# Optimization experiments

Measured on AMD Instinct MI355X. Metric: run time of the kernel, lower is better.

Reference implementation:

```python
import jax, jax.numpy as jnp
import numpy as np

N, H, W = 131072, 28, 28


def _mute(x):
    """Vectorized mute_bit: m,e = frexp(x); e = 0 if e > 1 else e; ldexp(m, e).
    Equivalent to scaling x by 2**(-e) when e > 1, identity otherwise.
    frexp's integer exponent carries no gradient, so this is also vjp-safe."""
    e = jnp.frexp(x)[1]                      # integer exponent, frexp convention: x = m * 2**e, m in [0.5,1)
    shift = jnp.where(e > 1, -e, 0).astype(x.dtype)
    return x * jnp.exp2(shift)


def setup_inputs() -> dict:
    key = jax.random.key(0)
    kx, = jax.random.split(key, 1)
    # scale by 8 so a substantial fraction of elements have exponent > 1 (mute path fires)
    x = jax.random.normal(kx, (N, H, W), dtype=jnp.float32) * 8.0
    rows = jnp.array([0, 7, 14, 21], dtype=jnp.int32)
    cols = jnp.array([3, 10, 17, 24], dtype=jnp.int32)
    return {"x": x, "rows": rows, "cols": cols}


def reference(x, rows, cols):
    # Mute selected full rows first (X[i][r][j] for j in 0..27), then selected full cols
    # (X[i][j][c] for j in 0..27) on the already-updated array, matching loop order.
    x = x.at[:, rows, :].set(_mute(x[:, rows, :]))
    x = x.at[:, :, cols].set(_mute(x[:, :, cols]))
    return x
```

## Files before the change

### kernel.cpp

```cpp
#include <hip/hip_runtime.h>

__device__ __forceinline__ float mute1(float v) {
    unsigned b = __float_as_uint(v);
    unsigned e = (b >> 23) & 0xffu;
    float m = __uint_as_float((b & 0x807FFFFFu) | 0x3F000000u);
    return (e >= 128u) ? m : v;
}

__global__ __launch_bounds__(256) void mute_kernel(
    const float4* __restrict__ x, float4* __restrict__ out,
    const int* __restrict__ rows, const int* __restrict__ cols, int n4)
{
    unsigned row_mask = (1u << rows[0]) | (1u << rows[1]) | (1u << rows[2]) | (1u << rows[3]);
    unsigned col_mask = (1u << cols[0]) | (1u << cols[1]) | (1u << cols[2]) | (1u << cols[3]);

    int i = blockIdx.x * 256 + threadIdx.x;
    if (i >= n4) return;

    unsigned q = (unsigned)i % 196u;
    unsigned h = q / 7u;
    unsigned w = (q - h * 7u) * 4u;

    unsigned sel = (((row_mask >> h) & 1u) ? 0xFu : 0u) | ((col_mask >> w) & 0xFu);

    float4 v = x[i];
    if (sel & 1u) v.x = mute1(v.x);
    if (sel & 2u) v.y = mute1(v.y);
    if (sel & 4u) v.z = mute1(v.z);
    if (sel & 8u) v.w = mute1(v.w);
    out[i] = v;
}

extern "C" void kernel_launch(void* const* d_in, const int* in_sizes, int n_in,
                              void* d_out, int out_size, void* d_ws, size_t ws_size,
                              hipStream_t stream) {
    const float* x   = (const float*)d_in[0];
    const int* rows  = (const int*)d_in[1];
    const int* cols  = (const int*)d_in[2];
    float* out       = (float*)d_out;

    int n  = in_sizes[0];
    int n4 = n / 4;
    int blocks = (n4 + 255) / 256;

    mute_kernel<<<blocks, 256, 0, stream>>>(
        (const float4*)x, (float4*)out, rows, cols, n4);
}
```

Before: 628.1 us.

## Use grid-stride loop with 7-way unrolled nontemporal loads and stores

Replaces the one-thread-per-float4 launch with a fixed 2048-block grid-stride loop. Each iteration issues seven independent nontemporal loads, then mutes, then issues seven nontemporal stores. The goal is more memory-level parallelism per thread and less cache pollution on a purely streaming copy. The mute test becomes branchless select logic. It risks lower occupancy from register pressure and a launch geometry tuned for this size.

```diff
diff --git a/kernel.cpp b/kernel.cpp
--- a/kernel.cpp
+++ b/kernel.cpp
@@ -1,34 +1,58 @@
 #include <hip/hip_runtime.h>
 
-__device__ __forceinline__ float mute1(float v) {
+__device__ __forceinline__ float mute1(float v, unsigned on) {
     unsigned b = __float_as_uint(v);
-    unsigned e = (b >> 23) & 0xffu;
     float m = __uint_as_float((b & 0x807FFFFFu) | 0x3F000000u);
-    return (e >= 128u) ? m : v;
+    return (on && ((b & 0x7F800000u) >= 0x40000000u)) ? m : v;
 }
 
-__global__ __launch_bounds__(256) void mute_kernel(
-    const float4* __restrict__ x, float4* __restrict__ out,
+typedef float f32x4 __attribute__((ext_vector_type(4)));
+
+__device__ __forceinline__ f32x4 mute4(f32x4 v, unsigned sel) {
+    v.x = mute1(v.x, sel & 1u);
+    v.y = mute1(v.y, sel & 2u);
+    v.z = mute1(v.z, sel & 4u);
+    v.w = mute1(v.w, sel & 8u);
+    return v;
+}
+
+__device__ __forceinline__ unsigned sel_for(unsigned q, unsigned row_mask, unsigned col_mask) {
+    unsigned h = q / 7u;
+    unsigned w = (q - h * 7u) * 4u;
+    return (((row_mask >> h) & 1u) ? 0xFu : 0u) | ((col_mask >> w) & 0xFu);
+}
+
+__global__ __launch_bounds__(256, 4) void mute_kernel(
+    const f32x4* __restrict__ x, f32x4* __restrict__ out,
     const int* __restrict__ rows, const int* __restrict__ cols, int n4)
 {
     unsigned row_mask = (1u << rows[0]) | (1u << rows[1]) | (1u << rows[2]) | (1u << rows[3]);
     unsigned col_mask = (1u << cols[0]) | (1u << cols[1]) | (1u << cols[2]) | (1u << cols[3]);
 
-    int i = blockIdx.x * 256 + threadIdx.x;
-    if (i >= n4) return;
+    const int stride = (int)(gridDim.x * 256u);
+    int i = (int)(blockIdx.x * 256u + threadIdx.x);
 
-    unsigned q = (unsigned)i % 196u;
-    unsigned h = q / 7u;
-    unsigned w = (q - h * 7u) * 4u;
-
-    unsigned sel = (((row_mask >> h) & 1u) ? 0xFu : 0u) | ((col_mask >> w) & 0xFu);
-
-    float4 v = x[i];
-    if (sel & 1u) v.x = mute1(v.x);
-    if (sel & 2u) v.y = mute1(v.y);
-    if (sel & 4u) v.z = mute1(v.z);
-    if (sel & 8u) v.w = mute1(v.w);
-    out[i] = v;
+    constexpr int U = 7;
+    for (; i + (U - 1) * stride < n4; i += U * stride) {
+        f32x4 v[U];
+        #pragma unroll
+        for (int u = 0; u < U; ++u)
+            v[u] = __builtin_nontemporal_load(&x[i + u * stride]);
+        #pragma unroll
+        for (int u = 0; u < U; ++u) {
+            unsigned q = (unsigned)(i + u * stride) % 196u;
+            v[u] = mute4(v[u], sel_for(q, row_mask, col_mask));
+        }
+        #pragma unroll
+        for (int u = 0; u < U; ++u)
+            __builtin_nontemporal_store(v[u], &out[i + u * stride]);
+    }
+    for (; i < n4; i += stride) {
+        unsigned q = (unsigned)i % 196u;
+        __builtin_nontemporal_store(
+            mute4(__builtin_nontemporal_load(&x[i]), sel_for(q, row_mask, col_mask)),
+            &out[i]);
+    }
 }
 
 extern "C" void kernel_launch(void* const* d_in, const int* in_sizes, int n_in,
@@ -41,8 +65,11 @@
 
     int n  = in_sizes[0];
     int n4 = n / 4;
-    int blocks = (n4 + 255) / 256;
+
+    int blocks = 2048;
+    int max_needed = (n4 + 255) / 256;
+    if (blocks > max_needed) blocks = max_needed;
 
     mute_kernel<<<blocks, 256, 0, stream>>>(
-        (const float4*)x, (float4*)out, rows, cols, n4);
+        (const f32x4*)x, (f32x4*)out, rows, cols, n4);
 }
```

Result: slower. 661.6 us (+5.3%).
